# Performance work log

Hardware: AMD Instinct MI355X
Metric: run time of the kernel (lower is better)

## Reference

```python
import jax, jax.numpy as jnp
import numpy as np

DIM = 768
HEADS = 12


def setup_inputs() -> dict:
    key = jax.random.key(0)
    k1, k2, k3, k4 = jax.random.split(key, 4)
    x = jax.random.normal(k1, (8, 1024, DIM), dtype=jnp.float32)
    # qkv: Linear(dim, 3*dim, bias=False); torch stores weight as (out, in), y = x @ W.T
    w_qkv = jax.random.normal(k2, (3 * DIM, DIM), dtype=jnp.float32) * (DIM ** -0.5)
    w_fc = jax.random.normal(k3, (DIM, DIM), dtype=jnp.float32) * (DIM ** -0.5)
    b_fc = jax.random.normal(k4, (DIM,), dtype=jnp.float32) * 0.02
    return {"x": x, "w_qkv": w_qkv, "w_fc": w_fc, "b_fc": b_fc}


def reference(x, w_qkv, w_fc, b_fc):
    b, n, dim = x.shape
    h = HEADS
    d = dim // h
    qkv = jnp.einsum('bnd,ed->bne', x, w_qkv)  # [b, n, 3*dim]
    q, k, v = jnp.split(qkv, 3, axis=-1)
    # b n (h d) -> b h n d
    q = q.reshape(b, n, h, d).transpose(0, 2, 1, 3)
    k = k.reshape(b, n, h, d).transpose(0, 2, 1, 3)
    v = v.reshape(b, n, h, d).transpose(0, 2, 1, 3)
    # NOTE: original module computes d_k = dim**-0.5 but never applies it.
    scores = jnp.einsum('bhqd,bhkd->bhqk', q, k)  # unscaled, faithful to source
    attn = jax.nn.softmax(scores, axis=-1)
    out = jnp.einsum('bhqk,bhkd->bhqd', attn, v)
    out = out.transpose(0, 2, 1, 3).reshape(b, n, dim)  # b h n d -> b n (h d)
    out = jnp.einsum('bnd,ed->bne', out, w_fc) + b_fc
    return out
```

## Files before the change

kernel.cpp:

```cpp
#include <hip/hip_runtime.h>
#include <cstdint>
#include <cstddef>

typedef __bf16 bf16;
typedef __bf16 bf16x4 __attribute__((ext_vector_type(4)));
typedef __bf16 bf16x8 __attribute__((ext_vector_type(8)));
typedef float f32x4 __attribute__((ext_vector_type(4)));
typedef float f32x16 __attribute__((ext_vector_type(16)));

typedef const __attribute__((address_space(1))) void* gas_ptr;
typedef __attribute__((address_space(3))) void* las_ptr;

#define GLOAD_LDS16(g, l) __builtin_amdgcn_global_load_lds((gas_ptr)(g), (las_ptr)(l), 16, 0, 0)

__global__ void cvt_f32_bf16(const float* __restrict__ in, bf16* __restrict__ out, int n4) {
  int i = blockIdx.x * blockDim.x + threadIdx.x;
  int stride = gridDim.x * blockDim.x;
  for (; i < n4; i += stride) {
    float4 v = reinterpret_cast<const float4*>(in)[i];
    bf16x4 o;
    o[0] = (bf16)v.x; o[1] = (bf16)v.y; o[2] = (bf16)v.z; o[3] = (bf16)v.w;
    reinterpret_cast<bf16x4*>(out)[i] = o;
  }
}

template <int MODE>
__global__ __launch_bounds__(256, 3) void gemm_bt(
    const bf16* __restrict__ A, const bf16* __restrict__ B,
    int M, int N, int K,
    bf16* __restrict__ outb, float* __restrict__ outf,
    const float* __restrict__ bias) {
  constexpr int BK = 32;
  __shared__ bf16 ldsA[3][4096];
  __shared__ bf16 ldsB[3][4096];
  const int tid = threadIdx.x;
  const int l = tid & 63;
  const int w = tid >> 6;
  const int wr = w >> 1, wc = w & 1;
  const int lr = l & 15, lg = l >> 4;

  const int gx = gridDim.x;
  const int bid = blockIdx.y * gx + blockIdx.x;
  const int xcd = bid & 7, c = bid >> 3, rpx = gx >> 3;
  const int brow = (xcd * rpx + (c & (rpx - 1))) * 128;
  const int bcol = (c / rpx) * 128;

  const bf16* sa0 = A + (size_t)(brow + w * 16 + lr) * K + lg * 8;
  const bf16* sa1 = sa0 + (size_t)64 * K;
  const bf16* sb0 = B + (size_t)(bcol + w * 16 + lr) * K + lg * 8;
  const bf16* sb1 = sb0 + (size_t)64 * K;
  const int d0 = w * 512 + l * 8;
  const int d1 = (4 + w) * 512 + l * 8;

  f32x4 acc[4][4] = {};

  GLOAD_LDS16(sa0, &ldsA[0][d0]);
  GLOAD_LDS16(sa1, &ldsA[0][d1]);
  GLOAD_LDS16(sb0, &ldsB[0][d0]);
  GLOAD_LDS16(sb1, &ldsB[0][d1]);
  GLOAD_LDS16(sa0 + BK, &ldsA[1][d0]);
  GLOAD_LDS16(sa1 + BK, &ldsA[1][d1]);
  GLOAD_LDS16(sb0 + BK, &ldsB[1][d0]);
  GLOAD_LDS16(sb1 + BK, &ldsB[1][d1]);

  int p = 0;
  for (int k0 = 0; k0 < K; k0 += BK) {
    asm volatile("s_waitcnt vmcnt(4)" ::: "memory");
    __builtin_amdgcn_sched_barrier(0);
    __builtin_amdgcn_s_barrier();
    __builtin_amdgcn_sched_barrier(0);

    int kn = k0 + 2 * BK;
    if (kn >= K) kn = k0;
    const int pt = (p >= 1) ? p - 1 : 2;
    GLOAD_LDS16(sa0 + kn, &ldsA[pt][d0]);
    GLOAD_LDS16(sa1 + kn, &ldsA[pt][d1]);
    GLOAD_LDS16(sb0 + kn, &ldsB[pt][d0]);
    GLOAD_LDS16(sb1 + kn, &ldsB[pt][d1]);

    bf16x8 af[4], bfr[4];
#pragma unroll
    for (int mi = 0; mi < 4; mi++)
      af[mi] = *reinterpret_cast<const bf16x8*>(&ldsA[p][(wr * 4 + mi) * 512 + l * 8]);
#pragma unroll
    for (int ni = 0; ni < 4; ni++)
      bfr[ni] = *reinterpret_cast<const bf16x8*>(&ldsB[p][(wc * 4 + ni) * 512 + l * 8]);
    __builtin_amdgcn_s_setprio(1);
#pragma unroll
    for (int mi = 0; mi < 4; mi++)
#pragma unroll
      for (int ni = 0; ni < 4; ni++)
        acc[mi][ni] = __builtin_amdgcn_mfma_f32_16x16x32_bf16(af[mi], bfr[ni], acc[mi][ni], 0, 0, 0);
    __builtin_amdgcn_s_setprio(0);
    p = (p == 2) ? 0 : p + 1;
  }

#pragma unroll
  for (int mi = 0; mi < 4; mi++) {
#pragma unroll
    for (int r = 0; r < 4; r++) {
      const int m = brow + wr * 64 + mi * 16 + lg * 4 + r;
#pragma unroll
      for (int ni = 0; ni < 4; ni++) {
        const int e = bcol + wc * 64 + ni * 16 + lr;
        const float v = acc[mi][ni][r];
        if (MODE == 1) {
          outf[(size_t)m * N + e] = v + bias[e];
        } else {
          outb[(size_t)m * N + e] = (bf16)v;
        }
      }
    }
  }
}

__global__ __launch_bounds__(256) void vtrans(const bf16* __restrict__ qkv,
                                              bf16* __restrict__ vtb) {
  __shared__ bf16 t[64 * 72];
  const int bh = blockIdx.x;
  const int b = bh / 12, h = bh % 12;
  const int nt = blockIdx.y;
  const int tid = threadIdx.x;
#pragma unroll
  for (int it = 0; it < 2; it++) {
    const int item = tid + it * 256;
    const int nl = item >> 3, c = item & 7;
    bf16x8 v = *reinterpret_cast<const bf16x8*>(
        &qkv[(size_t)(b * 1024 + nt * 64 + nl) * 2304 + 1536 + h * 64 + c * 8]);
#pragma unroll
    for (int j = 0; j < 8; j++) t[(c * 8 + j) * 72 + nl] = v[j];
  }
  __syncthreads();
#pragma unroll
  for (int it = 0; it < 2; it++) {
    const int item = tid + it * 256;
    const int d = item >> 3, c2 = item & 7;
    bf16x8 v = *reinterpret_cast<const bf16x8*>(&t[d * 72 + c2 * 8]);
    *reinterpret_cast<bf16x8*>(
        &vtb[(size_t)bh * 65536 + d * 1024 + nt * 64 + c2 * 8]) = v;
  }
}

__global__ __launch_bounds__(256, 3) void attn_kernel(
    const bf16* __restrict__ QKV, const bf16* __restrict__ Vt,
    bf16* __restrict__ Out) {
  __shared__ bf16 Kb[2][4096];
  __shared__ bf16 Vb[2][4096];
  const int tid = threadIdx.x;
  const int l = tid & 63;
  const int w = tid >> 6;
  const int ql = l & 31;
  const int hi = l >> 5;
  const int bh = blockIdx.x;
  const int b = bh / 12, h = bh % 12;
  const int q0 = blockIdx.y * 128 + w * 32;
  const bf16* Vh = Vt + (size_t)bh * 65536;
  constexpr float L2E = 1.4426950408889634f;

  const int kdst0 = (0 * 4 + w) * 512 + l * 8;
  const int kdst1 = (1 * 4 + w) * 512 + l * 8;
  const bf16* ksrc0 = QKV + (size_t)(b * 1024 + ql) * 2304 + 768 + h * 64 + w * 16 + hi * 8;
  const bf16* ksrc1 = ksrc0 + (size_t)32 * 2304;
  const bf16* vsrc0 = Vh + (size_t)((w & 1) * 32 + ql) * 1024 + ((0 * 4 + w) >> 1) * 16 + hi * 8;
  const bf16* vsrc1 = Vh + (size_t)((w & 1) * 32 + ql) * 1024 + ((1 * 4 + w) >> 1) * 16 + hi * 8;

  const bf16* Qrow = QKV + (size_t)(b * 1024 + q0 + ql) * 2304 + h * 64;
  bf16x8 qf[4];
#pragma unroll
  for (int s = 0; s < 4; s++)
    qf[s] = *reinterpret_cast<const bf16x8*>(&Qrow[s * 16 + hi * 8]);

  f32x16 o[2] = {};
  float ls0 = 0.f, ls1 = 0.f, ls2 = 0.f, ls3 = 0.f;

  GLOAD_LDS16(ksrc0, &Kb[0][kdst0]);
  GLOAD_LDS16(ksrc1, &Kb[0][kdst1]);
  GLOAD_LDS16(vsrc0, &Vb[0][kdst0]);
  GLOAD_LDS16(vsrc1, &Vb[0][kdst1]);
  asm volatile("s_waitcnt vmcnt(0)" ::: "memory");
  __syncthreads();

  int p = 0;
  for (int it = 0; it < 16; ++it) {
    const int kt = it * 64;
    if (it < 15) {
      GLOAD_LDS16(ksrc0 + (size_t)(kt + 64) * 2304, &Kb[p ^ 1][kdst0]);
      GLOAD_LDS16(ksrc1 + (size_t)(kt + 64) * 2304, &Kb[p ^ 1][kdst1]);
      GLOAD_LDS16(vsrc0 + (kt + 64), &Vb[p ^ 1][kdst0]);
      GLOAD_LDS16(vsrc1 + (kt + 64), &Vb[p ^ 1][kdst1]);
    }

    bf16x8 kf[8];
#pragma unroll
    for (int r = 0; r < 8; r++)
      kf[r] = *reinterpret_cast<const bf16x8*>(&Kb[p][r * 512 + l * 8]);
    f32x16 st0 = {}, st1 = {};
    __builtin_amdgcn_s_setprio(1);
#pragma unroll
    for (int s = 0; s < 4; s++) {
      st0 = __builtin_amdgcn_mfma_f32_32x32x16_bf16(kf[s], qf[s], st0, 0, 0, 0);
      st1 = __builtin_amdgcn_mfma_f32_32x32x16_bf16(kf[4 + s], qf[s], st1, 0, 0, 0);
    }
    __builtin_amdgcn_s_setprio(0);

#pragma unroll
    for (int r = 0; r < 16; r++) {
      float a0 = st0[r] * L2E, a1 = st1[r] * L2E;
      float e0, e1;
      asm("v_exp_f32 %0, %1" : "=v"(e0) : "v"(a0));
      asm("v_exp_f32 %0, %1" : "=v"(e1) : "v"(a1));
      st0[r] = e0; st1[r] = e1;
    }
#pragma unroll
    for (int r = 0; r < 16; r += 2) {
      ls0 += st0[r]; ls1 += st0[r + 1];
      ls2 += st1[r]; ls3 += st1[r + 1];
    }

    bf16x8 pfv[4];
#pragma unroll
    for (int t = 0; t < 4; t++) {
      const int c8 = (t & 1) * 8;
      const f32x16& sv = (t < 2) ? st0 : st1;
      uint32_t wA0, wA1, wB0, wB1;
      asm("v_cvt_pk_bf16_f32 %0, %1, %2" : "=v"(wA0) : "v"(sv[c8 + 0]), "v"(sv[c8 + 1]));
      asm("v_cvt_pk_bf16_f32 %0, %1, %2" : "=v"(wA1) : "v"(sv[c8 + 2]), "v"(sv[c8 + 3]));
      asm("v_cvt_pk_bf16_f32 %0, %1, %2" : "=v"(wB0) : "v"(sv[c8 + 4]), "v"(sv[c8 + 5]));
      asm("v_cvt_pk_bf16_f32 %0, %1, %2" : "=v"(wB1) : "v"(sv[c8 + 6]), "v"(sv[c8 + 7]));
      asm("v_permlane32_swap_b32 %0, %1" : "+v"(wA0), "+v"(wB0));
      asm("v_permlane32_swap_b32 %0, %1" : "+v"(wA1), "+v"(wB1));
      union { uint32_t u[4]; bf16x8 v; } pf;
      pf.u[0] = wA0; pf.u[1] = wA1; pf.u[2] = wB0; pf.u[3] = wB1;
      pfv[t] = pf.v;
    }

    bf16x8 vf[8];
#pragma unroll
    for (int r = 0; r < 8; r++)
      vf[r] = *reinterpret_cast<const bf16x8*>(&Vb[p][r * 512 + l * 8]);
    __builtin_amdgcn_s_setprio(1);
#pragma unroll
    for (int t = 0; t < 4; t++) {
      o[0] = __builtin_amdgcn_mfma_f32_32x32x16_bf16(vf[t * 2 + 0], pfv[t], o[0], 0, 0, 0);
      o[1] = __builtin_amdgcn_mfma_f32_32x32x16_bf16(vf[t * 2 + 1], pfv[t], o[1], 0, 0, 0);
    }
    __builtin_amdgcn_s_setprio(0);

    asm volatile("s_waitcnt vmcnt(0)" ::: "memory");
    __syncthreads();
    p ^= 1;
  }

  float lsum = (ls0 + ls1) + (ls2 + ls3);
  lsum += __shfl_xor(lsum, 32);
  const float rl = 1.0f / lsum;
  bf16* orow = Out + (size_t)(b * 1024 + q0 + ql) * 768 + h * 64;
#pragma unroll
  for (int dh = 0; dh < 2; dh++)
#pragma unroll
    for (int rq = 0; rq < 4; rq++) {
      union { ushort us[4]; uint2 v; } pk;
#pragma unroll
      for (int i = 0; i < 4; i++) {
        const bf16 hv = (bf16)(o[dh][rq * 4 + i] * rl);
        pk.us[i] = __builtin_bit_cast(ushort, hv);
      }
      *reinterpret_cast<uint2*>(&orow[dh * 32 + rq * 8 + hi * 4]) = pk.v;
    }
}

extern "C" void kernel_launch(void* const* d_in, const int* in_sizes, int n_in,
                              void* d_out, int out_size, void* d_ws, size_t ws_size,
                              hipStream_t stream) {
  const float* x = (const float*)d_in[0];
  const float* w_qkv = (const float*)d_in[1];
  const float* w_fc = (const float*)d_in[2];
  const float* b_fc = (const float*)d_in[3];
  float* out = (float*)d_out;
  char* ws = (char*)d_ws;

  bf16* xb = (bf16*)(ws);
  bf16* vtb = (bf16*)(ws);
  bf16* wqkb = (bf16*)(ws + 12582912);
  bf16* wfcb = (bf16*)(ws + 16121856);
  bf16* qkvb = (bf16*)(ws + 17301504);
  bf16* aob = (bf16*)(ws + 55050240);

  cvt_f32_bf16<<<2048, 256, 0, stream>>>(x, xb, 6291456 / 4);
  cvt_f32_bf16<<<1728, 256, 0, stream>>>(w_qkv, wqkb, 1769472 / 4);
  cvt_f32_bf16<<<576, 256, 0, stream>>>(w_fc, wfcb, 589824 / 4);

  gemm_bt<0><<<dim3(64, 18), 256, 0, stream>>>(xb, wqkb, 8192, 2304, 768,
                                               qkvb, nullptr, nullptr);

  vtrans<<<dim3(96, 16), 256, 0, stream>>>(qkvb, vtb);

  attn_kernel<<<dim3(96, 8), 256, 0, stream>>>(qkvb, vtb, aob);

  gemm_bt<1><<<dim3(64, 6), 256, 0, stream>>>(aob, wfcb, 8192, 768, 768,
                                              nullptr, out, b_fc);
}
```

Before: 156.1 us.

## Enlarge GEMM block tile to 256x128 with 8 waves and shared LDS buffer

Switches the bf16 GEMM from 128x128 tiles with 4 waves to 256x128 tiles with 8 waves, so each B tile in LDS is reused across twice as many rows. A and B stages are merged into one LDS array, the per-stage load count drops to three, and the XCD-aware block mapping is hardcoded for the new grid. It also drops the MFMA priority boost. The output-projection GEMM now launches only 192 blocks, which may underfill the GPU.

```diff
diff --git a/kernel.cpp b/kernel.cpp
--- a/kernel.cpp
+++ b/kernel.cpp
@@ -25,47 +25,43 @@
 }
 
 template <int MODE>
-__global__ __launch_bounds__(256, 3) void gemm_bt(
+__global__ __launch_bounds__(512, 4) void gemm_bt(
     const bf16* __restrict__ A, const bf16* __restrict__ B,
     int M, int N, int K,
     bf16* __restrict__ outb, float* __restrict__ outf,
     const float* __restrict__ bias) {
   constexpr int BK = 32;
-  __shared__ bf16 ldsA[3][4096];
-  __shared__ bf16 ldsB[3][4096];
+  __shared__ bf16 lds[3][12288];
   const int tid = threadIdx.x;
   const int l = tid & 63;
   const int w = tid >> 6;
   const int wr = w >> 1, wc = w & 1;
   const int lr = l & 15, lg = l >> 4;
 
-  const int gx = gridDim.x;
-  const int bid = blockIdx.y * gx + blockIdx.x;
-  const int xcd = bid & 7, c = bid >> 3, rpx = gx >> 3;
-  const int brow = (xcd * rpx + (c & (rpx - 1))) * 128;
-  const int bcol = (c / rpx) * 128;
+  const int bid = blockIdx.y * 32 + blockIdx.x;
+  const int xcd = bid & 7, c = bid >> 3;
+  const int brow = (xcd * 4 + (c & 3)) * 256;
+  const int bcol = (c >> 2) * 128;
 
   const bf16* sa0 = A + (size_t)(brow + w * 16 + lr) * K + lg * 8;
-  const bf16* sa1 = sa0 + (size_t)64 * K;
+  const bf16* sa1 = sa0 + (size_t)128 * K;
   const bf16* sb0 = B + (size_t)(bcol + w * 16 + lr) * K + lg * 8;
-  const bf16* sb1 = sb0 + (size_t)64 * K;
-  const int d0 = w * 512 + l * 8;
-  const int d1 = (4 + w) * 512 + l * 8;
+  const int dA0 = w * 512 + l * 8;
+  const int dA1 = (8 + w) * 512 + l * 8;
+  const int dB0 = 8192 + w * 512 + l * 8;
 
   f32x4 acc[4][4] = {};
 
-  GLOAD_LDS16(sa0, &ldsA[0][d0]);
-  GLOAD_LDS16(sa1, &ldsA[0][d1]);
-  GLOAD_LDS16(sb0, &ldsB[0][d0]);
-  GLOAD_LDS16(sb1, &ldsB[0][d1]);
-  GLOAD_LDS16(sa0 + BK, &ldsA[1][d0]);
-  GLOAD_LDS16(sa1 + BK, &ldsA[1][d1]);
-  GLOAD_LDS16(sb0 + BK, &ldsB[1][d0]);
-  GLOAD_LDS16(sb1 + BK, &ldsB[1][d1]);
+  GLOAD_LDS16(sa0, &lds[0][dA0]);
+  GLOAD_LDS16(sa1, &lds[0][dA1]);
+  GLOAD_LDS16(sb0, &lds[0][dB0]);
+  GLOAD_LDS16(sa0 + BK, &lds[1][dA0]);
+  GLOAD_LDS16(sa1 + BK, &lds[1][dA1]);
+  GLOAD_LDS16(sb0 + BK, &lds[1][dB0]);
 
   int p = 0;
   for (int k0 = 0; k0 < K; k0 += BK) {
-    asm volatile("s_waitcnt vmcnt(4)" ::: "memory");
+    asm volatile("s_waitcnt vmcnt(3)" ::: "memory");
     __builtin_amdgcn_sched_barrier(0);
     __builtin_amdgcn_s_barrier();
     __builtin_amdgcn_sched_barrier(0);
@@ -73,25 +69,22 @@
     int kn = k0 + 2 * BK;
     if (kn >= K) kn = k0;
     const int pt = (p >= 1) ? p - 1 : 2;
-    GLOAD_LDS16(sa0 + kn, &ldsA[pt][d0]);
-    GLOAD_LDS16(sa1 + kn, &ldsA[pt][d1]);
-    GLOAD_LDS16(sb0 + kn, &ldsB[pt][d0]);
-    GLOAD_LDS16(sb1 + kn, &ldsB[pt][d1]);
+    GLOAD_LDS16(sa0 + kn, &lds[pt][dA0]);
+    GLOAD_LDS16(sa1 + kn, &lds[pt][dA1]);
+    GLOAD_LDS16(sb0 + kn, &lds[pt][dB0]);
 
     bf16x8 af[4], bfr[4];
 #pragma unroll
     for (int mi = 0; mi < 4; mi++)
-      af[mi] = *reinterpret_cast<const bf16x8*>(&ldsA[p][(wr * 4 + mi) * 512 + l * 8]);
+      af[mi] = *reinterpret_cast<const bf16x8*>(&lds[p][(wr * 4 + mi) * 512 + l * 8]);
 #pragma unroll
     for (int ni = 0; ni < 4; ni++)
-      bfr[ni] = *reinterpret_cast<const bf16x8*>(&ldsB[p][(wc * 4 + ni) * 512 + l * 8]);
-    __builtin_amdgcn_s_setprio(1);
+      bfr[ni] = *reinterpret_cast<const bf16x8*>(&lds[p][8192 + (wc * 4 + ni) * 512 + l * 8]);
 #pragma unroll
     for (int mi = 0; mi < 4; mi++)
 #pragma unroll
       for (int ni = 0; ni < 4; ni++)
         acc[mi][ni] = __builtin_amdgcn_mfma_f32_16x16x32_bf16(af[mi], bfr[ni], acc[mi][ni], 0, 0, 0);
-    __builtin_amdgcn_s_setprio(0);
     p = (p == 2) ? 0 : p + 1;
   }
 
@@ -290,13 +283,13 @@
   cvt_f32_bf16<<<1728, 256, 0, stream>>>(w_qkv, wqkb, 1769472 / 4);
   cvt_f32_bf16<<<576, 256, 0, stream>>>(w_fc, wfcb, 589824 / 4);
 
-  gemm_bt<0><<<dim3(64, 18), 256, 0, stream>>>(xb, wqkb, 8192, 2304, 768,
+  gemm_bt<0><<<dim3(32, 18), 512, 0, stream>>>(xb, wqkb, 8192, 2304, 768,
                                                qkvb, nullptr, nullptr);
 
   vtrans<<<dim3(96, 16), 256, 0, stream>>>(qkvb, vtb);
 
   attn_kernel<<<dim3(96, 8), 256, 0, stream>>>(qkvb, vtb, aob);
 
-  gemm_bt<1><<<dim3(64, 6), 256, 0, stream>>>(aob, wfcb, 8192, 768, 768,
+  gemm_bt<1><<<dim3(32, 6), 512, 0, stream>>>(aob, wfcb, 8192, 768, 768,
                                               nullptr, out, b_fc);
 }
```

After: 145.0 us. 7.1% less time.
